# Kernel tuning notes

Hardware: AMD Instinct MI355X
Metric: run time of the kernel (lower is better)

The kernel has to match this reference:

```python
import jax, jax.numpy as jnp
import numpy as np

B, N, INDIM = 512, 200, 200
D1, D2, D3 = 32, 32, 8
RATIO = 0.5
K1 = int(np.ceil(RATIO * N))    # 100 nodes kept after pool1
K2 = int(np.ceil(RATIO * K1))   # 50 nodes kept after pool2
BN_EPS = 1e-5
NEG = -1e9


def setup_inputs() -> dict:
    key = jax.random.key(0)
    ks = jax.random.split(key, 16)
    x = jax.random.normal(ks[0], (B, N, INDIM), jnp.float32)
    u = jax.random.uniform(ks[1], (B, N, N), jnp.float32)
    ut = jnp.triu(jnp.where(u > 0.9, u, 0.0), 1)
    adj = ut + jnp.swapaxes(ut, 1, 2)
    g = lambda i, shape: jax.random.normal(ks[i], shape, jnp.float32) * 0.1
    return dict(
        x=x, adj=adj,
        W1=g(2, (INDIM, D1)), a1s=g(3, (D1,)), a1d=g(4, (D1,)), b1=jnp.zeros((D1,), jnp.float32),
        W2=g(5, (D1, D2)), a2s=g(6, (D2,)), a2d=g(7, (D2,)), b2=jnp.zeros((D2,), jnp.float32),
        pw1=g(8, (D1,)), pw2=g(9, (D2,)),
        fc1_w=g(10, ((D1 + D2) * 2, D2)), fc1_b=jnp.zeros((D2,), jnp.float32),
        fc2_w=g(11, (D2, D3)), fc2_b=jnp.zeros((D3,), jnp.float32),
        fc3_w=g(12, (D3, 2)), fc3_b=jnp.zeros((2,), jnp.float32),
        bn4_g=jnp.ones((D2,), jnp.float32), bn4_b=jnp.zeros((D2,), jnp.float32),
        bn5_g=jnp.ones((D3,), jnp.float32), bn5_b=jnp.zeros((D3,), jnp.float32))


def _gat(x, mask, W, a_s, a_d, b):
    # PyG GATConv (heads=1): alpha_ij = softmax_j LeakyReLU(a_d.h_i + a_s.h_j) over in-neighbors j (self-loops added)
    h = jnp.einsum('bnf,fd->bnd', x, W)
    es = h @ a_s                    # [B,n] source term
    ed = h @ a_d                    # [B,n] dest term
    m = mask | jnp.eye(mask.shape[1], dtype=bool)
    logits = jax.nn.leaky_relu(ed[:, :, None] + es[:, None, :], 0.2)
    alpha = jax.nn.softmax(jnp.where(m, logits, NEG), axis=-1)   # [B,n,n]
    return jnp.einsum('bij,bjd->bid', alpha, h) + b


def _topk(x, adj_w, w, k):
    # TopKPooling(multiplier=1, nonlinearity=sigmoid): score = sigmoid(x.w/||w||)
    score = jax.nn.sigmoid((x @ w) / (jnp.linalg.norm(w) + 1e-16))   # [B,n]
    vals, idx = jax.lax.top_k(score, k)                              # perm sorted desc, as PyG
    xk = jnp.take_along_axis(x, idx[:, :, None], axis=1) * vals[:, :, None]
    ak = jnp.take_along_axis(jnp.take_along_axis(adj_w, idx[:, :, None], axis=1), idx[:, None, :], axis=2)
    return xk, ak, vals


def _bn(z, g, b):
    # eval-mode BatchNorm1d: running_mean=0, running_var=1
    return g * z / jnp.sqrt(1.0 + BN_EPS) + b


def reference(x, adj, W1, a1s, a1d, b1, W2, a2s, a2d, b2, pw1, pw2,
              fc1_w, fc1_b, fc2_w, fc2_b, fc3_w, fc3_b, bn4_g, bn4_b, bn5_g, bn5_b):
    h = _gat(x, adj > 0, W1, a1s, a1d, b1)
    h, aw, s1 = _topk(h, adj, pw1, K1)
    x1 = jnp.concatenate([h.max(axis=1), h.mean(axis=1)], axis=1)    # [B, 64]
    # augment_adj: add self-loops, spspmm (A+I)@(A+I), remove self-loops
    eye = jnp.eye(K1, dtype=aw.dtype)
    a2 = jnp.einsum('bij,bjk->bik', aw + eye, aw + eye) * (1.0 - eye)
    h = _gat(h, a2 != 0, W2, a2s, a2d, b2)
    h, _, s2 = _topk(h, a2, pw2, K2)
    x2 = jnp.concatenate([h.max(axis=1), h.mean(axis=1)], axis=1)    # [B, 64]
    z = jnp.concatenate([x1, x2], axis=1)                            # [B, 128]
    z = _bn(jax.nn.relu(z @ fc1_w + fc1_b), bn4_g, bn4_b)            # dropout: eval -> identity
    z = _bn(jax.nn.relu(z @ fc2_w + fc2_b), bn5_g, bn5_b)
    logp = jax.nn.log_softmax(z @ fc3_w + fc3_b, axis=-1)            # [B, 2]
    return logp, s1, s2
```

## Files before the change

kernel.cpp:

```cpp
#include <hip/hip_runtime.h>
#include <math.h>

#define N_   200
#define B_   512
#define K1_  100
#define K2_  50

#define S1_OFF 1024
#define S2_OFF 52224

__device__ __forceinline__ float lrelu(float v) { return v > 0.f ? v : 0.2f * v; }
__device__ __forceinline__ float sigm(float v)  { return 1.f / (1.f + __expf(-v)); }

__device__ __forceinline__ void bitonic_desc(float* key, int* idx, int n, int t) {
  for (int k = 2; k <= n; k <<= 1) {
    for (int j = k >> 1; j > 0; j >>= 1) {
      __syncthreads();
      int ixj = t ^ j;
      if (t < n && ixj > t) {
        float a = key[t], c = key[ixj];
        int ia = idx[t], ic = idx[ixj];
        bool gt = (a > c) || (a == c && ia < ic);
        if (((t & k) == 0) ? !gt : gt) {
          key[t] = c; key[ixj] = a; idx[t] = ic; idx[ixj] = ia;
        }
      }
    }
  }
  __syncthreads();
}


__global__ __launch_bounds__(256) void gnn_fused(
    const float* __restrict__ x, const float* __restrict__ adj,
    const float* __restrict__ W1, const float* __restrict__ a1s,
    const float* __restrict__ a1d, const float* __restrict__ b1,
    const float* __restrict__ W2g, const float* __restrict__ a2s,
    const float* __restrict__ a2d, const float* __restrict__ b2,
    const float* __restrict__ pw1, const float* __restrict__ pw2,
    const float* __restrict__ fc1w, const float* __restrict__ fc1b,
    const float* __restrict__ fc2w, const float* __restrict__ fc2b,
    const float* __restrict__ fc3w, const float* __restrict__ fc3b,
    const float* __restrict__ bn4g, const float* __restrict__ bn4b,
    const float* __restrict__ bn5g, const float* __restrict__ bn5b,
    float* __restrict__ out)
{
  __shared__ __align__(16) char smem[64992];
  float*    sH    = (float*)smem;
  float*    sH1   = (float*)(smem + 25600);
  float*    sXK   = (float*)(smem + 38400);
  float*    sES   = (float*)(smem + 51200);
  float*    sED   = (float*)(smem + 52000);
  unsigned* sBITS = (unsigned*)(smem + 52800);
  float*    sW2   = (float*)(smem + 52800);
  float*    sKey  = (float*)(smem + 58400);
  int*      sIdx  = (int*)(smem + 59424);
  int*      sSel  = (int*)(smem + 60448);
  float*    sVal  = (float*)(smem + 60848);
  float*    sXV   = (float*)(smem + 61248);
  float*    sRed  = (float*)(smem + 61760);
  unsigned* sMask2= (unsigned*)(smem + 61792);

  const int t = threadIdx.x;
  const int b = blockIdx.x;
  const float* xb = x   + (size_t)b * N_ * N_;
  const float* ab = adj + (size_t)b * N_ * N_;

  for (int wi = t; wi < 1400; wi += 256) {
    int row = wi / 7;
    int w   = wi - row * 7;
    const float* p = ab + row * N_ + w * 32;
    unsigned m = 0u;
    const int lim = (w < 6) ? 32 : 8;
    for (int e = 0; e < lim; e += 4) {
      float4 v = *(const float4*)(p + e);
      m |= (unsigned)(v.x > 0.f) << e;
      m |= (unsigned)(v.y > 0.f) << (e + 1);
      m |= (unsigned)(v.z > 0.f) << (e + 2);
      m |= (unsigned)(v.w > 0.f) << (e + 3);
    }
    sBITS[row * 7 + w] = m;
  }

  if (t < N_) {
    float acc[32];
    #pragma unroll
    for (int d = 0; d < 32; ++d) acc[d] = 0.f;
    const float* xr = xb + t * N_;
    for (int k = 0; k < N_; k += 4) {
      float4 xv = *(const float4*)(xr + k);
      #pragma unroll
      for (int kk = 0; kk < 4; ++kk) {
        float xs = (&xv.x)[kk];
        const float* wr = W1 + (k + kk) * 32;
        #pragma unroll
        for (int d = 0; d < 32; ++d) acc[d] += xs * wr[d];
      }
    }
    float es = 0.f, ed = 0.f;
    #pragma unroll
    for (int d = 0; d < 32; ++d) { es += acc[d] * a1s[d]; ed += acc[d] * a1d[d]; }
    sES[t] = es; sED[t] = ed;
    #pragma unroll
    for (int d = 0; d < 32; ++d) sH[t * 32 + d] = acc[d];
  }
  __syncthreads();

  {
    float v = (t < N_) ? sES[t] : -3.0e38f;
    #pragma unroll
    for (int off = 1; off < 64; off <<= 1) v = fmaxf(v, __shfl_xor(v, off, 64));
    if ((t & 63) == 0) sRed[t >> 6] = v;
  }
  __syncthreads();
  {
    const float esmax = fmaxf(fmaxf(sRed[0], sRed[1]), fmaxf(sRed[2], sRed[3]));

    const int wv = t >> 6;
    const int lane = t & 63;
    const int dg = lane >> 4;
    const int rg = lane & 15;
    const int rbase = wv * 50;
    int   rowc[4]; bool val[4];
    float edv[4], Lv[4], ssum[4];
    float acc[4][8];
    #pragma unroll
    for (int rr = 0; rr < 4; ++rr) {
      int rl = rg + 16 * rr;
      val[rr] = rl < 50;
      rowc[rr] = val[rr] ? (rbase + rl) : 0;
      edv[rr] = sED[rowc[rr]];
      Lv[rr]  = lrelu(edv[rr] + esmax);
      ssum[rr] = 0.f;
      #pragma unroll
      for (int d = 0; d < 8; ++d) acc[rr][d] = 0.f;
    }
    for (int jw = 0; jw < 7; ++jw) {
      unsigned mw[4];
      #pragma unroll
      for (int rr = 0; rr < 4; ++rr) {
        mw[rr] = val[rr] ? sBITS[rowc[rr] * 7 + jw] : 0u;
        if (val[rr] && (rowc[rr] >> 5) == jw) mw[rr] |= 1u << (rowc[rr] & 31);
      }
      const int cnt = (jw < 6) ? 32 : 8;
      for (int jj4 = 0; jj4 < cnt; jj4 += 4) {
        float4 esv = *(const float4*)&sES[jw * 32 + jj4];
        #pragma unroll
        for (int u = 0; u < 4; ++u) {
          int jj = jj4 + u;
          int j = jw * 32 + jj;
          float esj = (&esv.x)[u];
          float4 h0 = *(const float4*)&sH[j * 32 + dg * 8];
          float4 h1v = *(const float4*)&sH[j * 32 + dg * 8 + 4];
          #pragma unroll
          for (int rr = 0; rr < 4; ++rr) {
            float w = ((mw[rr] >> jj) & 1u) ? __expf(lrelu(edv[rr] + esj) - Lv[rr]) : 0.f;
            ssum[rr] += w;
            acc[rr][0] += w * h0.x; acc[rr][1] += w * h0.y;
            acc[rr][2] += w * h0.z; acc[rr][3] += w * h0.w;
            acc[rr][4] += w * h1v.x; acc[rr][5] += w * h1v.y;
            acc[rr][6] += w * h1v.z; acc[rr][7] += w * h1v.w;
          }
        }
      }
    }
    float4 b1a = *(const float4*)(b1 + dg * 8);
    float4 b1b = *(const float4*)(b1 + dg * 8 + 4);
    #pragma unroll
    for (int rr = 0; rr < 4; ++rr) {
      if (val[rr]) {
        float inv = 1.f / ssum[rr];
        float4 o0, o1;
        o0.x = acc[rr][0] * inv + b1a.x; o0.y = acc[rr][1] * inv + b1a.y;
        o0.z = acc[rr][2] * inv + b1a.z; o0.w = acc[rr][3] * inv + b1a.w;
        o1.x = acc[rr][4] * inv + b1b.x; o1.y = acc[rr][5] * inv + b1b.y;
        o1.z = acc[rr][6] * inv + b1b.z; o1.w = acc[rr][7] * inv + b1b.w;
        *(float4*)&sH1[rowc[rr] * 32 + dg * 8]     = o0;
        *(float4*)&sH1[rowc[rr] * 32 + dg * 8 + 4] = o1;
      }
    }
  }
  __syncthreads();

  {
    float npw = 0.f;
    #pragma unroll
    for (int d = 0; d < 32; ++d) npw += pw1[d] * pw1[d];
    npw = sqrtf(npw) + 1e-16f;
    float sc = -1.f;
    if (t < N_) {
      float dp = 0.f;
      #pragma unroll
      for (int d = 0; d < 32; ++d) dp += sH1[t * 32 + d] * pw1[d];
      sc = sigm(dp / npw);
    }
    sKey[t] = sc; sIdx[t] = t;
  }
  bitonic_desc(sKey, sIdx, 256, t);
  if (t < K1_) {
    out[S1_OFF + b * K1_ + t] = sKey[t];
    sVal[t] = sKey[t]; sSel[t] = sIdx[t];
  }
  __syncthreads();
  {
    float tmp[13];
    #pragma unroll
    for (int it = 0; it < 13; ++it) {
      int i = t + it * 256;
      if (i < K1_ * 32) tmp[it] = sH1[sSel[i >> 5] * 32 + (i & 31)] * sVal[i >> 5];
    }
    __syncthreads();
    #pragma unroll
    for (int it = 0; it < 13; ++it) {
      int i = t + it * 256;
      if (i < K1_ * 32) sXK[i] = tmp[it];
    }
  }
  __syncthreads();
  if (t < 32) {
    float m = -3.0e38f, s = 0.f;
    for (int r = 0; r < K1_; ++r) { float v = sXK[r * 32 + t]; m = fmaxf(m, v); s += v; }
    sXV[t] = m; sXV[32 + t] = s / 100.f;
  }

  if (t < K1_) {
    int gi = sSel[t];
    unsigned bt[7];
    #pragma unroll
    for (int w = 0; w < 7; ++w) bt[w] = sBITS[gi * 7 + w];
    #pragma unroll
    for (int w = 0; w < 4; ++w) {
      unsigned m = 0;
      const int lim = (w < 3) ? 32 : 4;
      for (int jj = 0; jj < lim; ++jj) {
        int j = w * 32 + jj;
        int gj = sSel[j];
        unsigned bit = (bt[gj >> 5] >> (gj & 31)) & 1u;
        if (j == t) bit = 1u;
        m |= bit << jj;
      }
      sMask2[t * 8 + w] = m;
    }
  }
  __syncthreads();
  {
    unsigned pr0 = 0, pr1 = 0, pr2 = 0, pr3 = 0;
    unsigned ow0 = 0, ow1 = 0, ow2 = 0, ow3 = 0;
    if (t < K1_) {
      ow0 = sMask2[t * 8 + 0]; ow1 = sMask2[t * 8 + 1];
      ow2 = sMask2[t * 8 + 2]; ow3 = sMask2[t * 8 + 3];
    }
    for (int k = 0; k < K1_; ++k) {
      uint4 mk = *(const uint4*)&sMask2[k * 8];
      unsigned bit = (k < 32) ? (ow0 >> k) : (k < 64) ? (ow1 >> (k - 32))
                   : (k < 96) ? (ow2 >> (k - 64)) : (ow3 >> (k - 96));
      unsigned sel = (bit & 1u) ? 0xFFFFFFFFu : 0u;
      pr0 |= mk.x & sel; pr1 |= mk.y & sel; pr2 |= mk.z & sel; pr3 |= mk.w & sel;
    }
    __syncthreads();
    if (t < K1_) {
      sMask2[t * 8 + 0] = pr0; sMask2[t * 8 + 1] = pr1;
      sMask2[t * 8 + 2] = pr2; sMask2[t * 8 + 3] = pr3;
    }
  }
  __syncthreads();

  for (int i = t; i < 1024; i += 256) sW2[i] = W2g[i];
  __syncthreads();
  if (t < K1_) {
    float acc[32];
    #pragma unroll
    for (int d = 0; d < 32; ++d) acc[d] = 0.f;
    for (int k = 0; k < 32; ++k) {
      float xv = sXK[t * 32 + k];
      const float* wr = &sW2[k * 32];
      #pragma unroll
      for (int d = 0; d < 32; ++d) acc[d] += xv * wr[d];
    }
    float es = 0.f, ed = 0.f;
    #pragma unroll
    for (int d = 0; d < 32; ++d) { es += acc[d] * a2s[d]; ed += acc[d] * a2d[d]; }
    sES[t] = es; sED[t] = ed;
    #pragma unroll
    for (int d = 0; d < 32; ++d) sH[t * 32 + d] = acc[d];
  }
  __syncthreads();
  {
    float v = (t < K1_) ? sES[t] : -3.0e38f;
    #pragma unroll
    for (int off = 1; off < 64; off <<= 1) v = fmaxf(v, __shfl_xor(v, off, 64));
    if ((t & 63) == 0) sRed[t >> 6] = v;
  }
  __syncthreads();
  {
    const float esm2 = fmaxf(fmaxf(sRed[0], sRed[1]), fmaxf(sRed[2], sRed[3]));
    const int wv = t >> 6;
    const int lane = t & 63;
    const int dg = lane >> 4;
    const int rg = lane & 15;
    const int rbase = wv * 25;
    int   rowc[2]; bool val[2];
    float edv[2], Lv[2], ssum[2];
    float acc[2][8];
    #pragma unroll
    for (int rr = 0; rr < 2; ++rr) {
      int rl = rg + 16 * rr;
      val[rr] = rl < 25;
      rowc[rr] = val[rr] ? (rbase + rl) : 0;
      edv[rr] = sED[rowc[rr]];
      Lv[rr]  = lrelu(edv[rr] + esm2);
      ssum[rr] = 0.f;
      #pragma unroll
      for (int d = 0; d < 8; ++d) acc[rr][d] = 0.f;
    }
    for (int jw = 0; jw < 4; ++jw) {
      unsigned mw[2];
      #pragma unroll
      for (int rr = 0; rr < 2; ++rr)
        mw[rr] = val[rr] ? sMask2[rowc[rr] * 8 + jw] : 0u;
      const int cnt = (jw < 3) ? 32 : 4;
      for (int jj4 = 0; jj4 < cnt; jj4 += 4) {
        float4 esv = *(const float4*)&sES[jw * 32 + jj4];
        #pragma unroll
        for (int u = 0; u < 4; ++u) {
          int jj = jj4 + u;
          int j = jw * 32 + jj;
          float esj = (&esv.x)[u];
          float4 h0 = *(const float4*)&sH[j * 32 + dg * 8];
          float4 h1v = *(const float4*)&sH[j * 32 + dg * 8 + 4];
          #pragma unroll
          for (int rr = 0; rr < 2; ++rr) {
            float w = ((mw[rr] >> jj) & 1u) ? __expf(lrelu(edv[rr] + esj) - Lv[rr]) : 0.f;
            ssum[rr] += w;
            acc[rr][0] += w * h0.x; acc[rr][1] += w * h0.y;
            acc[rr][2] += w * h0.z; acc[rr][3] += w * h0.w;
            acc[rr][4] += w * h1v.x; acc[rr][5] += w * h1v.y;
            acc[rr][6] += w * h1v.z; acc[rr][7] += w * h1v.w;
          }
        }
      }
    }
    float4 b2a = *(const float4*)(b2 + dg * 8);
    float4 b2b = *(const float4*)(b2 + dg * 8 + 4);
    #pragma unroll
    for (int rr = 0; rr < 2; ++rr) {
      if (val[rr]) {
        float inv = 1.f / ssum[rr];
        float4 o0, o1;
        o0.x = acc[rr][0] * inv + b2a.x; o0.y = acc[rr][1] * inv + b2a.y;
        o0.z = acc[rr][2] * inv + b2a.z; o0.w = acc[rr][3] * inv + b2a.w;
        o1.x = acc[rr][4] * inv + b2b.x; o1.y = acc[rr][5] * inv + b2b.y;
        o1.z = acc[rr][6] * inv + b2b.z; o1.w = acc[rr][7] * inv + b2b.w;
        *(float4*)&sH1[rowc[rr] * 32 + dg * 8]     = o0;
        *(float4*)&sH1[rowc[rr] * 32 + dg * 8 + 4] = o1;
      }
    }
  }
  __syncthreads();

  {
    float npw = 0.f;
    #pragma unroll
    for (int d = 0; d < 32; ++d) npw += pw2[d] * pw2[d];
    npw = sqrtf(npw) + 1e-16f;
    float sc = -1.f;
    if (t < K1_) {
      float dp = 0.f;
      #pragma unroll
      for (int d = 0; d < 32; ++d) dp += sH1[t * 32 + d] * pw2[d];
      sc = sigm(dp / npw);
    }
    if (t < 128) { sKey[t] = sc; sIdx[t] = t; }
  }
  bitonic_desc(sKey, sIdx, 128, t);
  if (t < K2_) {
    out[S2_OFF + b * K2_ + t] = sKey[t];
    sVal[t] = sKey[t]; sSel[t] = sIdx[t];
  }
  __syncthreads();
  {
    int d = t & 31, r0 = t >> 5;
    for (int r = r0; r < K2_; r += 8) sXK[r * 32 + d] = sH1[sSel[r] * 32 + d] * sVal[r];
  }
  __syncthreads();
  if (t < 32) {
    float m = -3.0e38f, s = 0.f;
    for (int r = 0; r < K2_; ++r) { float v = sXK[r * 32 + t]; m = fmaxf(m, v); s += v; }
    sXV[64 + t] = m; sXV[96 + t] = s / 50.f;
  }
  __syncthreads();

  const float RS = 0.99999500003749969f;
  if (t < 32) {
    float z = fc1b[t];
    for (int k = 0; k < 128; ++k) z += sXV[k] * fc1w[k * 32 + t];
    z = fmaxf(z, 0.f);
    z = bn4g[t] * z * RS + bn4b[t];
    sKey[t] = z;
  }
  __syncthreads();
  if (t < 8) {
    float z = fc2b[t];
    for (int k = 0; k < 32; ++k) z += sKey[k] * fc2w[k * 8 + t];
    z = fmaxf(z, 0.f);
    z = bn5g[t] * z * RS + bn5b[t];
    sKey[32 + t] = z;
  }
  __syncthreads();
  if (t < 2) {
    float z = fc3b[t];
    for (int k = 0; k < 8; ++k) z += sKey[32 + k] * fc3w[k * 2 + t];
    sKey[40 + t] = z;
  }
  __syncthreads();
  if (t < 2) {
    float z0 = sKey[40], z1 = sKey[41];
    float m = fmaxf(z0, z1);
    float lse = m + logf(__expf(z0 - m) + __expf(z1 - m));
    out[b * 2 + t] = sKey[40 + t] - lse;
  }
}

extern "C" void kernel_launch(void* const* d_in, const int* in_sizes, int n_in,
                              void* d_out, int out_size, void* d_ws, size_t ws_size,
                              hipStream_t stream) {
  (void)in_sizes; (void)n_in; (void)d_ws; (void)ws_size; (void)out_size;
  const float* x    = (const float*)d_in[0];
  const float* adj  = (const float*)d_in[1];
  const float* W1   = (const float*)d_in[2];
  const float* a1s  = (const float*)d_in[3];
  const float* a1d  = (const float*)d_in[4];
  const float* b1   = (const float*)d_in[5];
  const float* W2   = (const float*)d_in[6];
  const float* a2s  = (const float*)d_in[7];
  const float* a2d  = (const float*)d_in[8];
  const float* b2   = (const float*)d_in[9];
  const float* pw1  = (const float*)d_in[10];
  const float* pw2  = (const float*)d_in[11];
  const float* fc1w = (const float*)d_in[12];
  const float* fc1b = (const float*)d_in[13];
  const float* fc2w = (const float*)d_in[14];
  const float* fc2b = (const float*)d_in[15];
  const float* fc3w = (const float*)d_in[16];
  const float* fc3b = (const float*)d_in[17];
  const float* bn4g = (const float*)d_in[18];
  const float* bn4b = (const float*)d_in[19];
  const float* bn5g = (const float*)d_in[20];
  const float* bn5b = (const float*)d_in[21];

  gnn_fused<<<B_, 256, 0, stream>>>(x, adj, W1, a1s, a1d, b1, W2, a2s, a2d, b2,
                                    pw1, pw2, fc1w, fc1b, fc2w, fc2b, fc3w, fc3b,
                                    bn4g, bn4b, bn5g, bn5b, (float*)d_out);
}
```

Before: 345.4 us.

## Split input projection and mask building into a wide prep kernel

Moves the x@W1 projection, attention source/dest scores and adjacency bitmask construction into a separate prep kernel with many small blocks, so the global-memory-bound work is spread across far more workgroups than the one-block-per-graph fused kernel. The main kernel then loads precomputed h, es, ed and bits from workspace. GAT outputs stay in registers, and top-k gathering uses an inverse-permutation scatter instead of an sH1 buffer, which shrinks shared memory and may raise occupancy. The cost is an extra launch and a round trip of intermediates through global memory.

```diff
diff --git a/kernel.cpp b/kernel.cpp
--- a/kernel.cpp
+++ b/kernel.cpp
@@ -8,6 +8,11 @@
 
 #define S1_OFF 1024
 #define S2_OFF 52224
+
+#define WS_H    0u
+#define WS_ES   13107200u
+#define WS_ED   13516800u
+#define WS_BITS 13926400u
 
 __device__ __forceinline__ float lrelu(float v) { return v > 0.f ? v : 0.2f * v; }
 __device__ __forceinline__ float sigm(float v)  { return 1.f / (1.f + __expf(-v)); }
@@ -30,13 +35,83 @@
   __syncthreads();
 }
 
-
-__global__ __launch_bounds__(256) void gnn_fused(
+__global__ __launch_bounds__(128) void prep(
     const float* __restrict__ x, const float* __restrict__ adj,
     const float* __restrict__ W1, const float* __restrict__ a1s,
-    const float* __restrict__ a1d, const float* __restrict__ b1,
-    const float* __restrict__ W2g, const float* __restrict__ a2s,
-    const float* __restrict__ a2d, const float* __restrict__ b2,
+    const float* __restrict__ a1d,
+    float* __restrict__ hg, float* __restrict__ esg, float* __restrict__ edg,
+    unsigned* __restrict__ bitsg)
+{
+  __shared__ __align__(16) float sX[32 * 200];
+  const int t = threadIdx.x;
+  const int blk = blockIdx.x;
+  if (blk < 3200) {
+    const int r0 = blk * 32;
+    const float4* src = (const float4*)(x + (size_t)r0 * 200);
+    float4* dst = (float4*)sX;
+    #pragma unroll
+    for (int i = 0; i < 13; ++i) {
+      int idx = t + i * 128;
+      if (idx < 1600) dst[idx] = src[idx];
+    }
+    __syncthreads();
+    const int rl = t >> 2;
+    const int dq = t & 3;
+    const float4* W14 = (const float4*)W1;
+    const float4* xr4 = (const float4*)(sX + rl * 200);
+    float4 a0 = make_float4(0.f, 0.f, 0.f, 0.f);
+    float4 a1 = make_float4(0.f, 0.f, 0.f, 0.f);
+    for (int k4 = 0; k4 < 50; ++k4) {
+      float4 xv = xr4[k4];
+      #pragma unroll
+      for (int kk = 0; kk < 4; ++kk) {
+        int k = k4 * 4 + kk;
+        float xs = (&xv.x)[kk];
+        float4 w0 = W14[k * 8 + dq * 2];
+        float4 w1 = W14[k * 8 + dq * 2 + 1];
+        a0.x += xs * w0.x; a0.y += xs * w0.y; a0.z += xs * w0.z; a0.w += xs * w0.w;
+        a1.x += xs * w1.x; a1.y += xs * w1.y; a1.z += xs * w1.z; a1.w += xs * w1.w;
+      }
+    }
+    const int r = r0 + rl;
+    float4* hg4 = (float4*)hg;
+    hg4[r * 8 + dq * 2]     = a0;
+    hg4[r * 8 + dq * 2 + 1] = a1;
+    float4 s0 = *(const float4*)(a1s + dq * 8);
+    float4 s1 = *(const float4*)(a1s + dq * 8 + 4);
+    float4 d0 = *(const float4*)(a1d + dq * 8);
+    float4 d1 = *(const float4*)(a1d + dq * 8 + 4);
+    float pes = a0.x*s0.x + a0.y*s0.y + a0.z*s0.z + a0.w*s0.w
+              + a1.x*s1.x + a1.y*s1.y + a1.z*s1.z + a1.w*s1.w;
+    float ped = a0.x*d0.x + a0.y*d0.y + a0.z*d0.z + a0.w*d0.w
+              + a1.x*d1.x + a1.y*d1.y + a1.z*d1.z + a1.w*d1.w;
+    pes += __shfl_xor(pes, 1, 64); pes += __shfl_xor(pes, 2, 64);
+    ped += __shfl_xor(ped, 1, 64); ped += __shfl_xor(ped, 2, 64);
+    if (dq == 0) { esg[r] = pes; edg[r] = ped; }
+  } else {
+    const int wg = (blk - 3200) * 128 + t;
+    const int row = wg / 7;
+    const int w = wg - row * 7;
+    const float* p = adj + (size_t)row * 200 + w * 32;
+    unsigned m = 0u;
+    const int lim = (w < 6) ? 32 : 8;
+    for (int e = 0; e < lim; e += 4) {
+      float4 v = *(const float4*)(p + e);
+      m |= (unsigned)(v.x > 0.f) << e;
+      m |= (unsigned)(v.y > 0.f) << (e + 1);
+      m |= (unsigned)(v.z > 0.f) << (e + 2);
+      m |= (unsigned)(v.w > 0.f) << (e + 3);
+    }
+    bitsg[wg] = m;
+  }
+}
+
+__global__ __launch_bounds__(256) void gnn_main(
+    const float* __restrict__ hg, const float* __restrict__ esg,
+    const float* __restrict__ edg, const unsigned* __restrict__ bitsg,
+    const float* __restrict__ b1, const float* __restrict__ W2g,
+    const float* __restrict__ a2s, const float* __restrict__ a2d,
+    const float* __restrict__ b2,
     const float* __restrict__ pw1, const float* __restrict__ pw2,
     const float* __restrict__ fc1w, const float* __restrict__ fc1b,
     const float* __restrict__ fc2w, const float* __restrict__ fc2b,
@@ -45,64 +120,36 @@
     const float* __restrict__ bn5g, const float* __restrict__ bn5b,
     float* __restrict__ out)
 {
-  __shared__ __align__(16) char smem[64992];
+  __shared__ __align__(16) char smem[50592];
   float*    sH    = (float*)smem;
-  float*    sH1   = (float*)(smem + 25600);
-  float*    sXK   = (float*)(smem + 38400);
-  float*    sES   = (float*)(smem + 51200);
-  float*    sED   = (float*)(smem + 52000);
-  unsigned* sBITS = (unsigned*)(smem + 52800);
-  float*    sW2   = (float*)(smem + 52800);
-  float*    sKey  = (float*)(smem + 58400);
-  int*      sIdx  = (int*)(smem + 59424);
-  int*      sSel  = (int*)(smem + 60448);
-  float*    sVal  = (float*)(smem + 60848);
-  float*    sXV   = (float*)(smem + 61248);
-  float*    sRed  = (float*)(smem + 61760);
-  unsigned* sMask2= (unsigned*)(smem + 61792);
+  unsigned* sBITS = (unsigned*)(smem + 25600);
+  float*    sW2   = (float*)(smem + 25600);
+  float*    sXK   = (float*)(smem + 31200);
+  float*    sES   = (float*)(smem + 44000);
+  float*    sED   = (float*)(smem + 44800);
+  float*    sKey  = (float*)(smem + 45600);
+  int*      sIdx  = (int*)(smem + 46624);
+  int*      sInv  = (int*)(smem + 46624);
+  int*      sSel  = (int*)(smem + 47648);
+  float*    sVal  = (float*)(smem + 48048);
+  float*    sXV   = (float*)(smem + 48448);
+  float*    sRed  = (float*)(smem + 48960);
+  unsigned* sMask2= (unsigned*)(smem + 48992);
 
   const int t = threadIdx.x;
   const int b = blockIdx.x;
-  const float* xb = x   + (size_t)b * N_ * N_;
-  const float* ab = adj + (size_t)b * N_ * N_;
-
-  for (int wi = t; wi < 1400; wi += 256) {
-    int row = wi / 7;
-    int w   = wi - row * 7;
-    const float* p = ab + row * N_ + w * 32;
-    unsigned m = 0u;
-    const int lim = (w < 6) ? 32 : 8;
-    for (int e = 0; e < lim; e += 4) {
-      float4 v = *(const float4*)(p + e);
-      m |= (unsigned)(v.x > 0.f) << e;
-      m |= (unsigned)(v.y > 0.f) << (e + 1);
-      m |= (unsigned)(v.z > 0.f) << (e + 2);
-      m |= (unsigned)(v.w > 0.f) << (e + 3);
-    }
-    sBITS[row * 7 + w] = m;
-  }
-
-  if (t < N_) {
-    float acc[32];
-    #pragma unroll
-    for (int d = 0; d < 32; ++d) acc[d] = 0.f;
-    const float* xr = xb + t * N_;
-    for (int k = 0; k < N_; k += 4) {
-      float4 xv = *(const float4*)(xr + k);
-      #pragma unroll
-      for (int kk = 0; kk < 4; ++kk) {
-        float xs = (&xv.x)[kk];
-        const float* wr = W1 + (k + kk) * 32;
-        #pragma unroll
-        for (int d = 0; d < 32; ++d) acc[d] += xs * wr[d];
-      }
-    }
-    float es = 0.f, ed = 0.f;
-    #pragma unroll
-    for (int d = 0; d < 32; ++d) { es += acc[d] * a1s[d]; ed += acc[d] * a1d[d]; }
-    sES[t] = es; sED[t] = ed;
-    #pragma unroll
-    for (int d = 0; d < 32; ++d) sH[t * 32 + d] = acc[d];
+
+  {
+    const float4* hsrc = (const float4*)(hg + (size_t)b * 6400);
+    float4* hdst = (float4*)sH;
+    for (int i = t; i < 1600; i += 256) hdst[i] = hsrc[i];
+    if (t < 50) {
+      ((float4*)sES)[t] = ((const float4*)(esg + b * 200))[t];
+      ((float4*)sED)[t] = ((const float4*)(edg + b * 200))[t];
+    }
+    const uint4* bsrc = (const uint4*)(bitsg + b * 1400);
+    uint4* bdst = (uint4*)sBITS;
+    for (int i = t; i < 350; i += 256) bdst[i] = bsrc[i];
   }
   __syncthreads();
 
@@ -113,34 +160,34 @@
     if ((t & 63) == 0) sRed[t >> 6] = v;
   }
   __syncthreads();
-  {
-    const float esmax = fmaxf(fmaxf(sRed[0], sRed[1]), fmaxf(sRed[2], sRed[3]));
-
-    const int wv = t >> 6;
-    const int lane = t & 63;
-    const int dg = lane >> 4;
-    const int rg = lane & 15;
+  const float esmax = fmaxf(fmaxf(sRed[0], sRed[1]), fmaxf(sRed[2], sRed[3]));
+
+  const int wv = t >> 6, lane = t & 63;
+  const int dg = lane >> 4, rg = lane & 15;
+  float h1v[4][8]; float ssum1[4]; float edv1[4], Lv1[4];
+  int rowc1[4]; bool val1[4];
+  float b1c[8];
+  *(float4*)&b1c[0] = *(const float4*)(b1 + dg * 8);
+  *(float4*)&b1c[4] = *(const float4*)(b1 + dg * 8 + 4);
+  {
     const int rbase = wv * 50;
-    int   rowc[4]; bool val[4];
-    float edv[4], Lv[4], ssum[4];
-    float acc[4][8];
     #pragma unroll
     for (int rr = 0; rr < 4; ++rr) {
       int rl = rg + 16 * rr;
-      val[rr] = rl < 50;
-      rowc[rr] = val[rr] ? (rbase + rl) : 0;
-      edv[rr] = sED[rowc[rr]];
-      Lv[rr]  = lrelu(edv[rr] + esmax);
-      ssum[rr] = 0.f;
-      #pragma unroll
-      for (int d = 0; d < 8; ++d) acc[rr][d] = 0.f;
+      val1[rr] = rl < 50;
+      rowc1[rr] = val1[rr] ? (rbase + rl) : 0;
+      edv1[rr] = sED[rowc1[rr]];
+      Lv1[rr]  = lrelu(edv1[rr] + esmax);
+      ssum1[rr] = 0.f;
+      #pragma unroll
+      for (int u = 0; u < 8; ++u) h1v[rr][u] = 0.f;
     }
     for (int jw = 0; jw < 7; ++jw) {
       unsigned mw[4];
       #pragma unroll
       for (int rr = 0; rr < 4; ++rr) {
-        mw[rr] = val[rr] ? sBITS[rowc[rr] * 7 + jw] : 0u;
-        if (val[rr] && (rowc[rr] >> 5) == jw) mw[rr] |= 1u << (rowc[rr] & 31);
+        mw[rr] = val1[rr] ? sBITS[rowc1[rr] * 7 + jw] : 0u;
+        if (val1[rr] && (rowc1[rr] >> 5) == jw) mw[rr] |= 1u << (rowc1[rr] & 31);
       }
       const int cnt = (jw < 6) ? 32 : 8;
       for (int jj4 = 0; jj4 < cnt; jj4 += 4) {
@@ -151,50 +198,46 @@
           int j = jw * 32 + jj;
           float esj = (&esv.x)[u];
           float4 h0 = *(const float4*)&sH[j * 32 + dg * 8];
-          float4 h1v = *(const float4*)&sH[j * 32 + dg * 8 + 4];
+          float4 h1x = *(const float4*)&sH[j * 32 + dg * 8 + 4];
           #pragma unroll
           for (int rr = 0; rr < 4; ++rr) {
-            float w = ((mw[rr] >> jj) & 1u) ? __expf(lrelu(edv[rr] + esj) - Lv[rr]) : 0.f;
-            ssum[rr] += w;
-            acc[rr][0] += w * h0.x; acc[rr][1] += w * h0.y;
-            acc[rr][2] += w * h0.z; acc[rr][3] += w * h0.w;
-            acc[rr][4] += w * h1v.x; acc[rr][5] += w * h1v.y;
-            acc[rr][6] += w * h1v.z; acc[rr][7] += w * h1v.w;
+            float w = ((mw[rr] >> jj) & 1u) ? __expf(lrelu(edv1[rr] + esj) - Lv1[rr]) : 0.f;
+            ssum1[rr] += w;
+            h1v[rr][0] += w * h0.x;  h1v[rr][1] += w * h0.y;
+            h1v[rr][2] += w * h0.z;  h1v[rr][3] += w * h0.w;
+            h1v[rr][4] += w * h1x.x; h1v[rr][5] += w * h1x.y;
+            h1v[rr][6] += w * h1x.z; h1v[rr][7] += w * h1x.w;
           }
         }
       }
     }
-    float4 b1a = *(const float4*)(b1 + dg * 8);
-    float4 b1b = *(const float4*)(b1 + dg * 8 + 4);
     #pragma unroll
     for (int rr = 0; rr < 4; ++rr) {
-      if (val[rr]) {
-        float inv = 1.f / ssum[rr];
-        float4 o0, o1;
-        o0.x = acc[rr][0] * inv + b1a.x; o0.y = acc[rr][1] * inv + b1a.y;
-        o0.z = acc[rr][2] * inv + b1a.z; o0.w = acc[rr][3] * inv + b1a.w;
-        o1.x = acc[rr][4] * inv + b1b.x; o1.y = acc[rr][5] * inv + b1b.y;
-        o1.z = acc[rr][6] * inv + b1b.z; o1.w = acc[rr][7] * inv + b1b.w;
-        *(float4*)&sH1[rowc[rr] * 32 + dg * 8]     = o0;
-        *(float4*)&sH1[rowc[rr] * 32 + dg * 8 + 4] = o1;
-      }
-    }
-  }
-  __syncthreads();
+      float inv = 1.f / ssum1[rr];
+      #pragma unroll
+      for (int u = 0; u < 8; ++u) h1v[rr][u] = h1v[rr][u] * inv + b1c[u];
+    }
+  }
 
   {
     float npw = 0.f;
     #pragma unroll
     for (int d = 0; d < 32; ++d) npw += pw1[d] * pw1[d];
     npw = sqrtf(npw) + 1e-16f;
-    float sc = -1.f;
-    if (t < N_) {
-      float dp = 0.f;
-      #pragma unroll
-      for (int d = 0; d < 32; ++d) dp += sH1[t * 32 + d] * pw1[d];
-      sc = sigm(dp / npw);
-    }
-    sKey[t] = sc; sIdx[t] = t;
+    float pwc[8];
+    *(float4*)&pwc[0] = *(const float4*)(pw1 + dg * 8);
+    *(float4*)&pwc[4] = *(const float4*)(pw1 + dg * 8 + 4);
+    sKey[t] = -1.f; sIdx[t] = t;
+    __syncthreads();
+    #pragma unroll
+    for (int rr = 0; rr < 4; ++rr) {
+      float p = 0.f;
+      #pragma unroll
+      for (int u = 0; u < 8; ++u) p += h1v[rr][u] * pwc[u];
+      p += __shfl_xor(p, 16, 64);
+      p += __shfl_xor(p, 32, 64);
+      if (dg == 0 && val1[rr]) sKey[rowc1[rr]] = sigm(p / npw);
+    }
   }
   bitonic_desc(sKey, sIdx, 256, t);
   if (t < K1_) {
@@ -202,21 +245,25 @@
     sVal[t] = sKey[t]; sSel[t] = sIdx[t];
   }
   __syncthreads();
-  {
-    float tmp[13];
-    #pragma unroll
-    for (int it = 0; it < 13; ++it) {
-      int i = t + it * 256;
-      if (i < K1_ * 32) tmp[it] = sH1[sSel[i >> 5] * 32 + (i & 31)] * sVal[i >> 5];
-    }
-    __syncthreads();
-    #pragma unroll
-    for (int it = 0; it < 13; ++it) {
-      int i = t + it * 256;
-      if (i < K1_ * 32) sXK[i] = tmp[it];
-    }
-  }
-  __syncthreads();
+  if (t < 200) sInv[t] = -1;
+  __syncthreads();
+  if (t < K1_) sInv[sSel[t]] = t;
+  __syncthreads();
+  #pragma unroll
+  for (int rr = 0; rr < 4; ++rr) {
+    if (val1[rr]) {
+      int rk = sInv[rowc1[rr]];
+      if (rk >= 0) {
+        float vm = sVal[rk];
+        float4 o0 = make_float4(h1v[rr][0]*vm, h1v[rr][1]*vm, h1v[rr][2]*vm, h1v[rr][3]*vm);
+        float4 o1 = make_float4(h1v[rr][4]*vm, h1v[rr][5]*vm, h1v[rr][6]*vm, h1v[rr][7]*vm);
+        *(float4*)&sXK[rk * 32 + dg * 8]     = o0;
+        *(float4*)&sXK[rk * 32 + dg * 8 + 4] = o1;
+      }
+    }
+  }
+  __syncthreads();
+
   if (t < 32) {
     float m = -3.0e38f, s = 0.f;
     for (int r = 0; r < K1_; ++r) { float v = sXK[r * 32 + t]; m = fmaxf(m, v); s += v; }
@@ -239,7 +286,7 @@
         if (j == t) bit = 1u;
         m |= bit << jj;
       }
-      sMask2[t * 8 + w] = m;
+      sMask2[t * 4 + w] = m;
     }
   }
   __syncthreads();
@@ -247,11 +294,11 @@
     unsigned pr0 = 0, pr1 = 0, pr2 = 0, pr3 = 0;
     unsigned ow0 = 0, ow1 = 0, ow2 = 0, ow3 = 0;
     if (t < K1_) {
-      ow0 = sMask2[t * 8 + 0]; ow1 = sMask2[t * 8 + 1];
-      ow2 = sMask2[t * 8 + 2]; ow3 = sMask2[t * 8 + 3];
+      ow0 = sMask2[t * 4 + 0]; ow1 = sMask2[t * 4 + 1];
+      ow2 = sMask2[t * 4 + 2]; ow3 = sMask2[t * 4 + 3];
     }
     for (int k = 0; k < K1_; ++k) {
-      uint4 mk = *(const uint4*)&sMask2[k * 8];
+      uint4 mk = *(const uint4*)&sMask2[k * 4];
       unsigned bit = (k < 32) ? (ow0 >> k) : (k < 64) ? (ow1 >> (k - 32))
                    : (k < 96) ? (ow2 >> (k - 64)) : (ow3 >> (k - 96));
       unsigned sel = (bit & 1u) ? 0xFFFFFFFFu : 0u;
@@ -259,8 +306,8 @@
     }
     __syncthreads();
     if (t < K1_) {
-      sMask2[t * 8 + 0] = pr0; sMask2[t * 8 + 1] = pr1;
-      sMask2[t * 8 + 2] = pr2; sMask2[t * 8 + 3] = pr3;
+      sMask2[t * 4 + 0] = pr0; sMask2[t * 4 + 1] = pr1;
+      sMask2[t * 4 + 2] = pr2; sMask2[t * 4 + 3] = pr3;
     }
   }
   __syncthreads();
@@ -271,18 +318,24 @@
     float acc[32];
     #pragma unroll
     for (int d = 0; d < 32; ++d) acc[d] = 0.f;
-    for (int k = 0; k < 32; ++k) {
-      float xv = sXK[t * 32 + k];
-      const float* wr = &sW2[k * 32];
-      #pragma unroll
-      for (int d = 0; d < 32; ++d) acc[d] += xv * wr[d];
+    const float4* xk4 = (const float4*)(sXK + t * 32);
+    for (int k4 = 0; k4 < 8; ++k4) {
+      float4 xv = xk4[k4];
+      #pragma unroll
+      for (int kk = 0; kk < 4; ++kk) {
+        float xs = (&xv.x)[kk];
+        const float* wr = &sW2[(k4 * 4 + kk) * 32];
+        #pragma unroll
+        for (int d = 0; d < 32; ++d) acc[d] += xs * wr[d];
+      }
     }
     float es = 0.f, ed = 0.f;
     #pragma unroll
     for (int d = 0; d < 32; ++d) { es += acc[d] * a2s[d]; ed += acc[d] * a2d[d]; }
     sES[t] = es; sED[t] = ed;
     #pragma unroll
-    for (int d = 0; d < 32; ++d) sH[t * 32 + d] = acc[d];
+    for (int d = 0; d < 32; d += 4)
+      *(float4*)&sH[t * 32 + d] = make_float4(acc[d], acc[d+1], acc[d+2], acc[d+3]);
   }
   __syncthreads();
   {
@@ -292,32 +345,31 @@
     if ((t & 63) == 0) sRed[t >> 6] = v;
   }
   __syncthreads();
-  {
-    const float esm2 = fmaxf(fmaxf(sRed[0], sRed[1]), fmaxf(sRed[2], sRed[3]));
-    const int wv = t >> 6;
-    const int lane = t & 63;
-    const int dg = lane >> 4;
-    const int rg = lane & 15;
+  const float esm2 = fmaxf(fmaxf(sRed[0], sRed[1]), fmaxf(sRed[2], sRed[3]));
+
+  float h2v[2][8]; float ssum2[2]; float edv2[2], Lv2[2];
+  int rowc2[2]; bool val2[2];
+  float b2c[8];
+  *(float4*)&b2c[0] = *(const float4*)(b2 + dg * 8);
+  *(float4*)&b2c[4] = *(const float4*)(b2 + dg * 8 + 4);
+  {
     const int rbase = wv * 25;
-    int   rowc[2]; bool val[2];
-    float edv[2], Lv[2], ssum[2];
-    float acc[2][8];
     #pragma unroll
     for (int rr = 0; rr < 2; ++rr) {
       int rl = rg + 16 * rr;
-      val[rr] = rl < 25;
-      rowc[rr] = val[rr] ? (rbase + rl) : 0;
-      edv[rr] = sED[rowc[rr]];
-      Lv[rr]  = lrelu(edv[rr] + esm2);
-      ssum[rr] = 0.f;
-      #pragma unroll
-      for (int d = 0; d < 8; ++d) acc[rr][d] = 0.f;
+      val2[rr] = rl < 25;
+      rowc2[rr] = val2[rr] ? (rbase + rl) : 0;
+      edv2[rr] = sED[rowc2[rr]];
+      Lv2[rr]  = lrelu(edv2[rr] + esm2);
+      ssum2[rr] = 0.f;
+      #pragma unroll
+      for (int u = 0; u < 8; ++u) h2v[rr][u] = 0.f;
     }
     for (int jw = 0; jw < 4; ++jw) {
       unsigned mw[2];
       #pragma unroll
       for (int rr = 0; rr < 2; ++rr)
-        mw[rr] = val[rr] ? sMask2[rowc[rr] * 8 + jw] : 0u;
+        mw[rr] = val2[rr] ? sMask2[rowc2[rr] * 4 + jw] : 0u;
       const int cnt = (jw < 3) ? 32 : 4;
       for (int jj4 = 0; jj4 < cnt; jj4 += 4) {
         float4 esv = *(const float4*)&sES[jw * 32 + jj4];
@@ -327,50 +379,46 @@
           int j = jw * 32 + jj;
           float esj = (&esv.x)[u];
           float4 h0 = *(const float4*)&sH[j * 32 + dg * 8];
-          float4 h1v = *(const float4*)&sH[j * 32 + dg * 8 + 4];
+          float4 h1x = *(const float4*)&sH[j * 32 + dg * 8 + 4];
           #pragma unroll
           for (int rr = 0; rr < 2; ++rr) {
-            float w = ((mw[rr] >> jj) & 1u) ? __expf(lrelu(edv[rr] + esj) - Lv[rr]) : 0.f;
-            ssum[rr] += w;
-            acc[rr][0] += w * h0.x; acc[rr][1] += w * h0.y;
-            acc[rr][2] += w * h0.z; acc[rr][3] += w * h0.w;
-            acc[rr][4] += w * h1v.x; acc[rr][5] += w * h1v.y;
-            acc[rr][6] += w * h1v.z; acc[rr][7] += w * h1v.w;
+            float w = ((mw[rr] >> jj) & 1u) ? __expf(lrelu(edv2[rr] + esj) - Lv2[rr]) : 0.f;
+            ssum2[rr] += w;
+            h2v[rr][0] += w * h0.x;  h2v[rr][1] += w * h0.y;
+            h2v[rr][2] += w * h0.z;  h2v[rr][3] += w * h0.w;
+            h2v[rr][4] += w * h1x.x; h2v[rr][5] += w * h1x.y;
+            h2v[rr][6] += w * h1x.z; h2v[rr][7] += w * h1x.w;
           }
         }
       }
     }
-    float4 b2a = *(const float4*)(b2 + dg * 8);
-    float4 b2b = *(const float4*)(b2 + dg * 8 + 4);
     #pragma unroll
     for (int rr = 0; rr < 2; ++rr) {
-      if (val[rr]) {
-        float inv = 1.f / ssum[rr];
-        float4 o0, o1;
-        o0.x = acc[rr][0] * inv + b2a.x; o0.y = acc[rr][1] * inv + b2a.y;
-        o0.z = acc[rr][2] * inv + b2a.z; o0.w = acc[rr][3] * inv + b2a.w;
-        o1.x = acc[rr][4] * inv + b2b.x; o1.y = acc[rr][5] * inv + b2b.y;
-        o1.z = acc[rr][6] * inv + b2b.z; o1.w = acc[rr][7] * inv + b2b.w;
-        *(float4*)&sH1[rowc[rr] * 32 + dg * 8]     = o0;
-        *(float4*)&sH1[rowc[rr] * 32 + dg * 8 + 4] = o1;
-      }
-    }
-  }
-  __syncthreads();
+      float inv = 1.f / ssum2[rr];
+      #pragma unroll
+      for (int u = 0; u < 8; ++u) h2v[rr][u] = h2v[rr][u] * inv + b2c[u];
+    }
+  }
 
   {
     float npw = 0.f;
     #pragma unroll
     for (int d = 0; d < 32; ++d) npw += pw2[d] * pw2[d];
     npw = sqrtf(npw) + 1e-16f;
-    float sc = -1.f;
-    if (t < K1_) {
-      float dp = 0.f;
-      #pragma unroll
-      for (int d = 0; d < 32; ++d) dp += sH1[t * 32 + d] * pw2[d];
-      sc = sigm(dp / npw);
-    }
-    if (t < 128) { sKey[t] = sc; sIdx[t] = t; }
+    float pwc[8];
+    *(float4*)&pwc[0] = *(const float4*)(pw2 + dg * 8);
+    *(float4*)&pwc[4] = *(const float4*)(pw2 + dg * 8 + 4);
+    if (t < 128) { sKey[t] = -1.f; sIdx[t] = t; }
+    __syncthreads();
+    #pragma unroll
+    for (int rr = 0; rr < 2; ++rr) {
+      float p = 0.f;
+      #pragma unroll
+      for (int u = 0; u < 8; ++u) p += h2v[rr][u] * pwc[u];
+      p += __shfl_xor(p, 16, 64);
+      p += __shfl_xor(p, 32, 64);
+      if (dg == 0 && val2[rr]) sKey[rowc2[rr]] = sigm(p / npw);
+    }
   }
   bitonic_desc(sKey, sIdx, 128, t);
   if (t < K2_) {
@@ -378,9 +426,22 @@
     sVal[t] = sKey[t]; sSel[t] = sIdx[t];
   }
   __syncthreads();
-  {
-    int d = t & 31, r0 = t >> 5;
-    for (int r = r0; r < K2_; r += 8) sXK[r * 32 + d] = sH1[sSel[r] * 32 + d] * sVal[r];
+  if (t < K1_) sInv[t] = -1;
+  __syncthreads();
+  if (t < K2_) sInv[sSel[t]] = t;
+  __syncthreads();
+  #pragma unroll
+  for (int rr = 0; rr < 2; ++rr) {
+    if (val2[rr]) {
+      int rk = sInv[rowc2[rr]];
+      if (rk >= 0) {
+        float vm = sVal[rk];
+        float4 o0 = make_float4(h2v[rr][0]*vm, h2v[rr][1]*vm, h2v[rr][2]*vm, h2v[rr][3]*vm);
+        float4 o1 = make_float4(h2v[rr][4]*vm, h2v[rr][5]*vm, h2v[rr][6]*vm, h2v[rr][7]*vm);
+        *(float4*)&sXK[rk * 32 + dg * 8]     = o0;
+        *(float4*)&sXK[rk * 32 + dg * 8 + 4] = o1;
+      }
+    }
   }
   __syncthreads();
   if (t < 32) {
@@ -424,7 +485,7 @@
 extern "C" void kernel_launch(void* const* d_in, const int* in_sizes, int n_in,
                               void* d_out, int out_size, void* d_ws, size_t ws_size,
                               hipStream_t stream) {
-  (void)in_sizes; (void)n_in; (void)d_ws; (void)ws_size; (void)out_size;
+  (void)in_sizes; (void)n_in; (void)ws_size; (void)out_size;
   const float* x    = (const float*)d_in[0];
   const float* adj  = (const float*)d_in[1];
   const float* W1   = (const float*)d_in[2];
@@ -448,7 +509,15 @@
   const float* bn5g = (const float*)d_in[20];
   const float* bn5b = (const float*)d_in[21];
 
-  gnn_fused<<<B_, 256, 0, stream>>>(x, adj, W1, a1s, a1d, b1, W2, a2s, a2d, b2,
-                                    pw1, pw2, fc1w, fc1b, fc2w, fc2b, fc3w, fc3b,
-                                    bn4g, bn4b, bn5g, bn5b, (float*)d_out);
+  char* ws = (char*)d_ws;
+  float*    hg    = (float*)(ws + WS_H);
+  float*    esg   = (float*)(ws + WS_ES);
+  float*    edg   = (float*)(ws + WS_ED);
+  unsigned* bitsg = (unsigned*)(ws + WS_BITS);
+
+  prep<<<8800, 128, 0, stream>>>(x, adj, W1, a1s, a1d, hg, esg, edg, bitsg);
+  gnn_main<<<B_, 256, 0, stream>>>(hg, esg, edg, bitsg,
+                                   b1, W2, a2s, a2d, b2, pw1, pw2,
+                                   fc1w, fc1b, fc2w, fc2b, fc3w, fc3b,
+                                   bn4g, bn4b, bn5g, bn5b, (float*)d_out);
 }
```

New measurement: 376.9 us. +9.1%, slower.
